# Kernel tuning notes

Hardware: AMD Instinct MI355X
Metric: run time of the kernel (lower is better)

Reference implementation:

```python
import jax, jax.numpy as jnp
import numpy as np

L = 5          # num_layer
H = 32         # num_heads (feature dim)
G = 32         # n_graph
NN = 256       # n_node per graph
KB = 8         # adjacency band half-width
N = G * (2 * (KB * NN - KB * (KB + 1) // 2))   # 128768 angle-graph nodes
E = N * 16                                      # 2060288 angle-graph edges
NRBF = 20
BN_EPS = 1e-5
GAMMA = 10.0


def _band_adj():
    i = np.arange(NN)
    d = np.abs(i[:, None] - i[None, :])
    a = (d <= KB) & (d > 0)
    return jnp.asarray(np.broadcast_to(a, (G, NN, NN)).copy())


def setup_inputs() -> dict:
    key = jax.random.key(0)
    ks = jax.random.split(key, 10)
    adj = _band_adj()
    x_mask = jnp.ones((G, NN), dtype=bool)
    x_3d = jax.random.uniform(ks[0], (N, 1), minval=0.8, maxval=1.8)
    edge_attr_3d = jax.random.uniform(ks[1], (E, 1), minval=0.0, maxval=float(np.pi))
    edge_index = jax.random.randint(ks[2], (2, E), 0, N)
    s1 = 1.0 / np.sqrt(NRBF)
    sH = 1.0 / np.sqrt(H)
    s2H = 1.0 / np.sqrt(2 * H)
    return {
        "x_3d": x_3d, "edge_attr_3d": edge_attr_3d,
        "edge_index": edge_index, "adj": adj, "x_mask": x_mask,
        "w_len": jax.random.normal(ks[3], (NRBF, H)) * s1, "b_len": jnp.zeros(H),
        "w_ang": jax.random.normal(ks[4], (NRBF, H)) * s1, "b_ang": jnp.zeros(H),
        "w1": jax.random.normal(ks[5], (L, H, 2 * H)) * sH, "b1": jnp.zeros((L, 2 * H)),
        "bn1_g": jnp.ones((L, 2 * H)), "bn1_b": jnp.zeros((L, 2 * H)),
        "w2": jax.random.normal(ks[6], (L, 2 * H, H)) * s2H, "b2": jnp.zeros((L, H)),
        "eps_gin": jnp.zeros(L),
        "bn_g": jnp.ones((L, H)), "bn_b": jnp.zeros((L, H)),
        "ln_g": jnp.ones(H), "ln_b": jnp.zeros(H),
    }


def _bn(h, g, b):
    # BatchNorm1d in training mode (batch statistics)
    m = jnp.mean(h, axis=0)
    v = jnp.var(h, axis=0)
    return (h - m) * jax.lax.rsqrt(v + BN_EPS) * g + b


def _rbf(x, centers):
    # x: [M,1] -> [M, NRBF]
    return jnp.exp(-GAMMA * (x - centers) ** 2)


def _forward(x_3d, edge_attr_3d, edge_index, adj,
             w_len, b_len, w_ang, b_ang,
             w1, b1, bn1_g, bn1_b, w2, b2, eps_gin, bn_g, bn_b, ln_g, ln_b):
    cen_len = jnp.arange(NRBF, dtype=x_3d.dtype) * 0.1           # bond length RBF centers
    cen_ang = jnp.linspace(0.0, np.pi, NRBF).astype(x_3d.dtype)  # bond angle RBF centers
    x = _rbf(x_3d, cen_len) @ w_len + b_len                      # [N,H]
    ea = _rbf(edge_attr_3d, cen_ang) @ w_ang + b_ang             # [E,H]
    src, dst = edge_index[0], edge_index[1]

    h = x
    for l in range(L):
        # GINConvBondAngle: message = relu(x_j + edge_attr); aggr = add
        msg = jax.nn.relu(h[src] + ea)                           # [E,H]
        agg = jax.ops.segment_sum(msg, dst, num_segments=N)      # [N,H]
        z = (1.0 + eps_gin[l]) * h + agg
        z = _bn(z @ w1[l] + b1[l], bn1_g[l], bn1_b[l])           # mlp Linear+BN
        z = jax.nn.relu(z) @ w2[l] + b2[l]                       # mlp ReLU+Linear
        h = _bn(z, bn_g[l], bn_b[l])                             # outer batch norm
        if l != L - 1:
            h = jax.nn.relu(h)
        # dropout p=0 -> identity; residual=False; JK='last'

    mu = jnp.mean(h, axis=-1, keepdims=True)
    var = jnp.var(h, axis=-1, keepdims=True)
    nr = (h - mu) * jax.lax.rsqrt(var + BN_EPS) * ln_g + ln_b    # LayerNorm, [N,H]

    # masked dense scatter into [G*NN*NN, H]
    eye = jnp.eye(NN, dtype=bool)
    mask = (adj & ~eye).reshape(-1)                              # exactly N Trues
    pos = jnp.cumsum(mask) - 1                                   # row in nr for each True
    out = jnp.where(mask[:, None], nr[jnp.clip(pos, 0, N - 1)], 0.0)
    return out.reshape(G, NN, NN, H).transpose(0, 3, 1, 2)       # [G,H,NN,NN]


def reference(x_3d, edge_attr_3d, edge_index, adj, x_mask,
              w_len, b_len, w_ang, b_ang,
              w1, b1, bn1_g, bn1_b, w2, b2, eps_gin, bn_g, bn_b, ln_g, ln_b):
    return _forward(x_3d, edge_attr_3d, edge_index, adj,
                    w_len, b_len, w_ang, b_ang,
                    w1, b1, bn1_g, bn1_b, w2, b2, eps_gin, bn_g, bn_b, ln_g, ln_b)
```

## Files before the change

### kernel.cpp

```cpp
#include <hip/hip_runtime.h>
#include <hip/hip_bf16.h>

using bf16 = __hip_bfloat16;

#define HH 32
#define HH2 64
#define NRBF_ 20
#define NL 5
#define NNN 256
#define KBW 8
#define PGN 4024
#define TTAB 4096
constexpr int NNODE = 128768;
constexpr int NEDGE = 2060288;
constexpr float BNEPS = 1e-5f;
constexpr float PI_F = 3.14159265358979323846f;

__global__ void __launch_bounds__(256) k_node_embed(const float* __restrict__ x3d,
                                                    const float* __restrict__ wlen,
                                                    const float* __restrict__ blen,
                                                    float* __restrict__ hbuf) {
  __shared__ float wl[NRBF_ * HH];
  __shared__ float bl[HH];
  int t = threadIdx.x;
  for (int j = t; j < NRBF_ * HH; j += 256) wl[j] = wlen[j];
  if (t < HH) bl[t] = blen[t];
  __syncthreads();
  int idx = blockIdx.x * 256 + t;
  int n = idx >> 5, c = idx & 31;
  float x = x3d[n];
  float acc = bl[c];
#pragma unroll
  for (int k = 0; k < NRBF_; ++k) {
    float d = x - 0.1f * (float)k;
    acc = fmaf(__expf(-10.f * d * d), wl[k * HH + c], acc);
  }
  hbuf[idx] = acc;
}

__global__ void __launch_bounds__(256) k_tab(const float* __restrict__ wang,
                                             const float* __restrict__ bang,
                                             float* __restrict__ tab) {
  __shared__ float wa[NRBF_ * HH];
  __shared__ float ba[HH];
  int t = threadIdx.x;
  for (int j = t; j < NRBF_ * HH; j += 256) wa[j] = wang[j];
  if (t < HH) ba[t] = bang[t];
  __syncthreads();
  int idx = blockIdx.x * 256 + t;
  int row = idx >> 5, c = idx & 31;
  float ang = (float)row * (PI_F / (float)(TTAB - 1));
  const float step = PI_F / 19.f;
  float acc = ba[c];
#pragma unroll
  for (int k = 0; k < NRBF_; ++k) {
    float d = ang - step * (float)k;
    acc = fmaf(__expf(-10.f * d * d), wa[k * HH + c], acc);
  }
  tab[row * HH + c] = acc;
}

__global__ void __launch_bounds__(256) k_hist(const int* __restrict__ dst, int* __restrict__ counts) {
  int e = blockIdx.x * 256 + threadIdx.x;
  atomicAdd(&counts[dst[e]], 1);
}

__global__ void __launch_bounds__(256) k_scan1(const int* __restrict__ counts, int* __restrict__ bsum) {
  __shared__ int sd[256];
  int t = threadIdx.x;
  sd[t] = counts[blockIdx.x * 256 + t];
  __syncthreads();
  for (int s = 128; s > 0; s >>= 1) { if (t < s) sd[t] += sd[t + s]; __syncthreads(); }
  if (t == 0) bsum[blockIdx.x] = sd[0];
}

__global__ void __launch_bounds__(512) k_scan2(const int* __restrict__ bsum, int* __restrict__ boff) {
  __shared__ int sd[512];
  int t = threadIdx.x;
  int v = (t < 503) ? bsum[t] : 0;
  sd[t] = v;
  __syncthreads();
  for (int off = 1; off < 512; off <<= 1) {
    int x = (t >= off) ? sd[t - off] : 0;
    __syncthreads();
    sd[t] += x;
    __syncthreads();
  }
  if (t < 503) boff[t] = sd[t] - v;
}

__global__ void __launch_bounds__(256) k_scan3(const int* __restrict__ counts, const int* __restrict__ boff,
                                               int* __restrict__ rowptr, int* __restrict__ cursor) {
  __shared__ int sd[256];
  int t = threadIdx.x;
  int i = blockIdx.x * 256 + t;
  int v = counts[i];
  sd[t] = v;
  __syncthreads();
  for (int off = 1; off < 256; off <<= 1) {
    int x = (t >= off) ? sd[t - off] : 0;
    __syncthreads();
    sd[t] += x;
    __syncthreads();
  }
  int excl = sd[t] - v + boff[blockIdx.x];
  rowptr[i] = excl;
  cursor[i] = excl;
  if (i == NNODE - 1) rowptr[NNODE] = excl + v;
}

__global__ void __launch_bounds__(256) k_scatter(const int* __restrict__ srcA,
                                                 const int* __restrict__ dstA,
                                                 const float* __restrict__ eattr,
                                                 int* __restrict__ cursor,
                                                 int2* __restrict__ pk) {
  int bid = blockIdx.x;
  int x = bid & 7;
  int j = bid >> 3;
  int lo = x * (NNODE / 8);
  int hi = lo + (NNODE / 8);
  int e0 = j * 2048 + threadIdx.x;
#pragma unroll
  for (int k = 0; k < 8; ++k) {
    int e = e0 + k * 256;
    int d = dstA[e];
    if (d >= lo && d < hi) {
      int pos = atomicAdd(&cursor[d], 1);
      pk[pos] = make_int2(srcA[e], __float_as_int(eattr[e]));
    }
  }
}

__global__ void __launch_bounds__(256) k_layerA(const float* __restrict__ hbuf,
                                                const int* __restrict__ rowptr,
                                                const int2* __restrict__ pk,
                                                const float* __restrict__ tab,
                                                const float* __restrict__ statsC,
                                                const float* __restrict__ bng,
                                                const float* __restrict__ bnb,
                                                const float* __restrict__ w1g,
                                                const float* __restrict__ b1g,
                                                const float* __restrict__ epsg,
                                                float* __restrict__ y1buf,
                                                float* __restrict__ statsA,
                                                int l, int relu) {
  __shared__ float w1s[HH * HH2];
  __shared__ float b1s[HH2];
  __shared__ float affs[HH], affsh[HH];
  __shared__ float tb[8][HH + 1];
  __shared__ float ps[HH2], pq[HH2];
  int t = threadIdx.x;
  const float* w1l = w1g + l * HH * HH2;
  for (int j = t; j < HH * HH2; j += 256) w1s[j] = w1l[j];
  if (t < HH2) { b1s[t] = b1g[l * HH2 + t]; ps[t] = 0.f; pq[t] = 0.f; }
  if (t < HH) {
    if (l == 0) { affs[t] = 1.f; affsh[t] = 0.f; }
    else {
      float sum = statsC[(l - 1) * 64 + t], sq = statsC[(l - 1) * 64 + 32 + t];
      float mean = sum / (float)NNODE;
      float var = fmaxf(sq / (float)NNODE - mean * mean, 0.f);
      float s = bng[(l - 1) * HH + t] * rsqrtf(var + BNEPS);
      affs[t] = s; affsh[t] = bnb[(l - 1) * HH + t] - mean * s;
    }
  }
  int g = t >> 5, c = t & 31;
  float epsv = 1.f + epsg[l];
  float lo = relu ? 0.f : -3.4e38f;
  const float angsc = (float)(TTAB - 1) / PI_F;
  float s0a = 0.f, s0q = 0.f, s1a = 0.f, s1q = 0.f;
  __syncthreads();
  float sc = affs[c], sh = affsh[c];
  int stride = gridDim.x * 8;
  int iters = (NNODE + stride - 1) / stride;
  int n = blockIdx.x * 8 + g;
  for (int it = 0; it < iters; ++it, n += stride) {
    bool val = n < NNODE;
    float tv = 0.f;
    if (val) {
      int p0 = rowptr[n], p1 = rowptr[n + 1];
      float hn = fmaxf(fmaf(hbuf[n * HH + c], sc, sh), lo);
      float acc = 0.f;
      int p = p0;
      for (; p + 8 <= p1; p += 8) {
        int2 q0 = pk[p], q1 = pk[p + 1], q2 = pk[p + 2], q3 = pk[p + 3];
        int2 q4 = pk[p + 4], q5 = pk[p + 5], q6 = pk[p + 6], q7 = pk[p + 7];
        float h0 = hbuf[q0.x * HH + c], h1 = hbuf[q1.x * HH + c];
        float h2 = hbuf[q2.x * HH + c], h3 = hbuf[q3.x * HH + c];
        float h4 = hbuf[q4.x * HH + c], h5 = hbuf[q5.x * HH + c];
        float h6 = hbuf[q6.x * HH + c], h7 = hbuf[q7.x * HH + c];
        int i0 = min((int)fmaf(__int_as_float(q0.y), angsc, 0.5f), TTAB - 1);
        int i1 = min((int)fmaf(__int_as_float(q1.y), angsc, 0.5f), TTAB - 1);
        int i2 = min((int)fmaf(__int_as_float(q2.y), angsc, 0.5f), TTAB - 1);
        int i3 = min((int)fmaf(__int_as_float(q3.y), angsc, 0.5f), TTAB - 1);
        int i4 = min((int)fmaf(__int_as_float(q4.y), angsc, 0.5f), TTAB - 1);
        int i5 = min((int)fmaf(__int_as_float(q5.y), angsc, 0.5f), TTAB - 1);
        int i6 = min((int)fmaf(__int_as_float(q6.y), angsc, 0.5f), TTAB - 1);
        int i7 = min((int)fmaf(__int_as_float(q7.y), angsc, 0.5f), TTAB - 1);
        float e0 = tab[i0 * HH + c], e1 = tab[i1 * HH + c];
        float e2 = tab[i2 * HH + c], e3 = tab[i3 * HH + c];
        float e4 = tab[i4 * HH + c], e5 = tab[i5 * HH + c];
        float e6 = tab[i6 * HH + c], e7 = tab[i7 * HH + c];
        h0 = fmaxf(fmaf(h0, sc, sh), lo); h1 = fmaxf(fmaf(h1, sc, sh), lo);
        h2 = fmaxf(fmaf(h2, sc, sh), lo); h3 = fmaxf(fmaf(h3, sc, sh), lo);
        h4 = fmaxf(fmaf(h4, sc, sh), lo); h5 = fmaxf(fmaf(h5, sc, sh), lo);
        h6 = fmaxf(fmaf(h6, sc, sh), lo); h7 = fmaxf(fmaf(h7, sc, sh), lo);
        acc += fmaxf(h0 + e0, 0.f) + fmaxf(h1 + e1, 0.f) + fmaxf(h2 + e2, 0.f) + fmaxf(h3 + e3, 0.f)
             + fmaxf(h4 + e4, 0.f) + fmaxf(h5 + e5, 0.f) + fmaxf(h6 + e6, 0.f) + fmaxf(h7 + e7, 0.f);
      }
      for (; p < p1; ++p) {
        int2 q0 = pk[p];
        float h0 = fmaxf(fmaf(hbuf[q0.x * HH + c], sc, sh), lo);
        int i0 = min((int)fmaf(__int_as_float(q0.y), angsc, 0.5f), TTAB - 1);
        acc += fmaxf(h0 + tab[i0 * HH + c], 0.f);
      }
      tv = fmaf(epsv, hn, acc);
    }
    tb[g][c] = tv;
    __builtin_amdgcn_wave_barrier();
    if (val) {
      float y0 = b1s[c], y1 = b1s[HH + c];
#pragma unroll
      for (int k = 0; k < HH; ++k) {
        float tk = tb[g][k];
        y0 = fmaf(tk, w1s[k * HH2 + c], y0);
        y1 = fmaf(tk, w1s[k * HH2 + HH + c], y1);
      }
      y1buf[n * HH2 + c] = y0;
      y1buf[n * HH2 + HH + c] = y1;
      s0a += y0; s0q += y0 * y0; s1a += y1; s1q += y1 * y1;
    }
    __builtin_amdgcn_wave_barrier();
  }
  s0a += __shfl_xor(s0a, 32); s0q += __shfl_xor(s0q, 32);
  s1a += __shfl_xor(s1a, 32); s1q += __shfl_xor(s1q, 32);
  if ((t & 32) == 0) {
    atomicAdd(&ps[c], s0a); atomicAdd(&pq[c], s0q);
    atomicAdd(&ps[HH + c], s1a); atomicAdd(&pq[HH + c], s1q);
  }
  __syncthreads();
  if (t < HH2) {
    atomicAdd(&statsA[l * 128 + t], ps[t]);
    atomicAdd(&statsA[l * 128 + 64 + t], pq[t]);
  }
}

__global__ void __launch_bounds__(256) k_layerC(const float* __restrict__ y1buf,
                                                const float* __restrict__ statsA,
                                                const float* __restrict__ g1,
                                                const float* __restrict__ bb1,
                                                const float* __restrict__ w2g,
                                                const float* __restrict__ b2g,
                                                float* __restrict__ hbuf,
                                                float* __restrict__ statsC, int l) {
  __shared__ float w2s[HH2 * HH];
  __shared__ float b2s[HH];
  __shared__ float a1s[HH2], a1sh[HH2];
  __shared__ float ab[8][HH2 + 1];
  __shared__ float ps[HH], pq[HH];
  int t = threadIdx.x;
  const float* w2l = w2g + l * HH2 * HH;
  for (int j = t; j < HH2 * HH; j += 256) w2s[j] = w2l[j];
  if (t < HH) { b2s[t] = b2g[l * HH + t]; ps[t] = 0.f; pq[t] = 0.f; }
  if (t < HH2) {
    float sum = statsA[l * 128 + t], sq = statsA[l * 128 + 64 + t];
    float mean = sum / (float)NNODE;
    float var = fmaxf(sq / (float)NNODE - mean * mean, 0.f);
    float s = g1[l * HH2 + t] * rsqrtf(var + BNEPS);
    a1s[t] = s; a1sh[t] = bb1[l * HH2 + t] - mean * s;
  }
  int g = t >> 5, c = t & 31;
  float sa = 0.f, sq = 0.f;
  __syncthreads();
  int stride = gridDim.x * 8;
  int iters = (NNODE + stride - 1) / stride;
  int n = blockIdx.x * 8 + g;
  for (int it = 0; it < iters; ++it, n += stride) {
    bool val = n < NNODE;
    float a0 = 0.f, a1 = 0.f;
    if (val) {
      a0 = fmaf(y1buf[n * HH2 + c], a1s[c], a1sh[c]);
      a1 = fmaf(y1buf[n * HH2 + HH + c], a1s[HH + c], a1sh[HH + c]);
    }
    ab[g][c] = fmaxf(a0, 0.f);
    ab[g][HH + c] = fmaxf(a1, 0.f);
    __builtin_amdgcn_wave_barrier();
    if (val) {
      float z = b2s[c];
#pragma unroll
      for (int k = 0; k < HH2; ++k) z = fmaf(ab[g][k], w2s[k * HH + c], z);
      hbuf[n * HH + c] = z;
      sa += z; sq += z * z;
    }
    __builtin_amdgcn_wave_barrier();
  }
  sa += __shfl_xor(sa, 32); sq += __shfl_xor(sq, 32);
  if ((t & 32) == 0) { atomicAdd(&ps[c], sa); atomicAdd(&pq[c], sq); }
  __syncthreads();
  if (t < HH) {
    atomicAdd(&statsC[l * 64 + t], ps[t]);
    atomicAdd(&statsC[l * 64 + 32 + t], pq[t]);
  }
}

__global__ void __launch_bounds__(256) k_output(const float* __restrict__ hbuf,
                                                const float* __restrict__ statsC,
                                                const float* __restrict__ bng,
                                                const float* __restrict__ bnb,
                                                const float* __restrict__ lng,
                                                const float* __restrict__ lnb,
                                                float* __restrict__ out) {
  __shared__ float nrb[16 * 33];
  __shared__ float affs[HH], affsh[HH];
  int t = threadIdx.x;
  if (t < HH) {
    float sum = statsC[(NL - 1) * 64 + t], sq = statsC[(NL - 1) * 64 + 32 + t];
    float mean = sum / (float)NNODE;
    float var = fmaxf(sq / (float)NNODE - mean * mean, 0.f);
    float s = bng[(NL - 1) * HH + t] * rsqrtf(var + BNEPS);
    affs[t] = s; affsh[t] = bnb[(NL - 1) * HH + t] - mean * s;
  }
  __syncthreads();
  int gi = blockIdx.x;
  int g = gi >> 8, i = gi & 255;
  int jlo = (i - KBW > 0) ? i - KBW : 0;
  int jhi = (i + KBW < NNN - 1) ? i + KBW : NNN - 1;
  int cnt = jhi - jlo;
  int Ai = (i <= 8) ? i * (i - 1) / 2 : 28 + 8 * (i - 8);
  int Bi = (i <= 248) ? 8 * i : 2012 - (256 - i) * (255 - i) / 2;
  int nb = g * PGN + Ai + Bi;
  int r = t >> 5, c = t & 31;
  float sc = affs[c], sh = affsh[c];
  float lg = lng[c], lb = lnb[c];
  for (int rr = r; rr < cnt; rr += 8) {
    float v = fmaf(hbuf[(nb + rr) * HH + c], sc, sh);
    float s = v;
#pragma unroll
    for (int off = 16; off > 0; off >>= 1) s += __shfl_xor(s, off, 32);
    float mean = s * (1.f / 32.f);
    float d = v - mean;
    float q = d * d;
#pragma unroll
    for (int off = 16; off > 0; off >>= 1) q += __shfl_xor(q, off, 32);
    float var = q * (1.f / 32.f);
    nrb[rr * 33 + c] = d * rsqrtf(var + BNEPS) * lg + lb;
  }
  __syncthreads();
  int j = t;
  bool valid = (j >= jlo) & (j <= jhi) & (j != i);
  int rr = j - jlo - ((j > i) ? 1 : 0);
  rr = (rr < 0) ? 0 : ((rr > 15) ? 15 : rr);
  size_t ob = (((size_t)g * HH) * NNN + i) * NNN + j;
#pragma unroll
  for (int h = 0; h < HH; ++h) {
    float val = valid ? nrb[rr * 33 + h] : 0.f;
    __builtin_nontemporal_store(val, &out[ob + (size_t)h * NNN * NNN]);
  }
}

extern "C" void kernel_launch(void* const* d_in, const int* in_sizes, int n_in,
                              void* d_out, int out_size, void* d_ws, size_t ws_size,
                              hipStream_t stream) {
  (void)in_sizes; (void)n_in;
  const float* x3d   = (const float*)d_in[0];
  const float* eattr = (const float*)d_in[1];
  const int*   eidx  = (const int*)d_in[2];
  const float* wlen = (const float*)d_in[5];
  const float* blen = (const float*)d_in[6];
  const float* wang = (const float*)d_in[7];
  const float* bang = (const float*)d_in[8];
  const float* w1g  = (const float*)d_in[9];
  const float* b1g  = (const float*)d_in[10];
  const float* g1   = (const float*)d_in[11];
  const float* bb1  = (const float*)d_in[12];
  const float* w2g  = (const float*)d_in[13];
  const float* b2g  = (const float*)d_in[14];
  const float* epsg = (const float*)d_in[15];
  const float* bng  = (const float*)d_in[16];
  const float* bnb  = (const float*)d_in[17];
  const float* lng  = (const float*)d_in[18];
  const float* lnb  = (const float*)d_in[19];
  float* out = (float*)d_out;

  char* ws = (char*)d_ws;
  size_t off = 0;
  auto alloc = [&](size_t bytes) {
    void* p = ws + off;
    off += (bytes + 255) & ~(size_t)255;
    return p;
  };
  int2*  pk         = (int2*)alloc((size_t)NEDGE * 8);
  int*   rowptr     = (int*)alloc((size_t)(NNODE + 1) * 4);
  int*   counts     = (int*)alloc((size_t)NNODE * 4);
  int*   cursor     = (int*)alloc((size_t)NNODE * 4);
  float* hbuf       = (float*)alloc((size_t)NNODE * HH * 4);
  float* y1buf      = (float*)alloc((size_t)NNODE * HH2 * 4);
  float* tab        = (float*)alloc((size_t)TTAB * HH * 4);
  float* statsA     = (float*)alloc(NL * 128 * 4);
  float* statsC     = (float*)alloc(NL * 64 * 4);
  int*   bsum       = (int*)alloc(503 * 4);
  int*   boff       = (int*)alloc(503 * 4);

  if (off > ws_size) {
    hipMemsetAsync(d_out, 0x7F, (size_t)out_size * 4, stream);
    return;
  }

  hipMemsetAsync(counts, 0, (size_t)NNODE * 4, stream);
  hipMemsetAsync(statsA, 0, NL * 128 * 4, stream);
  hipMemsetAsync(statsC, 0, NL * 64 * 4, stream);

  k_node_embed<<<NNODE * HH / 256, 256, 0, stream>>>(x3d, wlen, blen, hbuf);
  k_tab<<<TTAB * HH / 256, 256, 0, stream>>>(wang, bang, tab);
  k_hist<<<NEDGE / 256, 256, 0, stream>>>(eidx + NEDGE, counts);
  k_scan1<<<NNODE / 256, 256, 0, stream>>>(counts, bsum);
  k_scan2<<<1, 512, 0, stream>>>(bsum, boff);
  k_scan3<<<NNODE / 256, 256, 0, stream>>>(counts, boff, rowptr, cursor);
  k_scatter<<<8048, 256, 0, stream>>>(eidx, eidx + NEDGE, eattr, cursor, pk);

  for (int l = 0; l < NL; ++l) {
    k_layerA<<<2048, 256, 0, stream>>>(hbuf, rowptr, pk, tab, statsC, bng, bnb,
                                       w1g, b1g, epsg, y1buf, statsA, l, l >= 1 ? 1 : 0);
    k_layerC<<<2048, 256, 0, stream>>>(y1buf, statsA, g1, bb1, w2g, b2g, hbuf, statsC, l);
  }

  k_output<<<NNN * 32, 256, 0, stream>>>(hbuf, statsC, bng, bnb, lng, lnb, out);
}
```

Measured before the change: 1.124 ms.

## Store node features, angle table, and MLP activations in fp16; pack edge records

Node features, the angle embedding table and the first-MLP activations are now stored as fp16 instead of fp32. Edge records are packed into one 32-bit word holding a 17-bit source index and a precomputed 12-bit table index, and are read with nontemporal loads. The goal is to cut the memory traffic of the gather-heavy aggregation and of the layer passes. The cost is reduced precision in intermediate activations, and the packing assumes fewer than 2^17 nodes.

```diff
diff --git a/kernel.cpp b/kernel.cpp
--- a/kernel.cpp
+++ b/kernel.cpp
@@ -1,7 +1,6 @@
 #include <hip/hip_runtime.h>
 #include <hip/hip_bf16.h>
-
-using bf16 = __hip_bfloat16;
+#include <hip/hip_fp16.h>
 
 #define HH 32
 #define HH2 64
@@ -19,7 +18,7 @@
 __global__ void __launch_bounds__(256) k_node_embed(const float* __restrict__ x3d,
                                                     const float* __restrict__ wlen,
                                                     const float* __restrict__ blen,
-                                                    float* __restrict__ hbuf) {
+                                                    __half* __restrict__ hbuf) {
   __shared__ float wl[NRBF_ * HH];
   __shared__ float bl[HH];
   int t = threadIdx.x;
@@ -35,12 +34,12 @@
     float d = x - 0.1f * (float)k;
     acc = fmaf(__expf(-10.f * d * d), wl[k * HH + c], acc);
   }
-  hbuf[idx] = acc;
+  hbuf[idx] = __float2half(acc);
 }
 
 __global__ void __launch_bounds__(256) k_tab(const float* __restrict__ wang,
                                              const float* __restrict__ bang,
-                                             float* __restrict__ tab) {
+                                             __half* __restrict__ tab) {
   __shared__ float wa[NRBF_ * HH];
   __shared__ float ba[HH];
   int t = threadIdx.x;
@@ -57,7 +56,7 @@
     float d = ang - step * (float)k;
     acc = fmaf(__expf(-10.f * d * d), wa[k * HH + c], acc);
   }
-  tab[row * HH + c] = acc;
+  tab[row * HH + c] = __float2half(acc);
 }
 
 __global__ void __launch_bounds__(256) k_hist(const int* __restrict__ dst, int* __restrict__ counts) {
@@ -113,7 +112,8 @@
                                                  const int* __restrict__ dstA,
                                                  const float* __restrict__ eattr,
                                                  int* __restrict__ cursor,
-                                                 int2* __restrict__ pk) {
+                                                 unsigned int* __restrict__ pk) {
+  const float angsc = (float)(TTAB - 1) / PI_F;
   int bid = blockIdx.x;
   int x = bid & 7;
   int j = bid >> 3;
@@ -126,22 +126,23 @@
     int d = dstA[e];
     if (d >= lo && d < hi) {
       int pos = atomicAdd(&cursor[d], 1);
-      pk[pos] = make_int2(srcA[e], __float_as_int(eattr[e]));
-    }
-  }
-}
-
-__global__ void __launch_bounds__(256) k_layerA(const float* __restrict__ hbuf,
+      unsigned int idx = min((unsigned int)fmaf(eattr[e], angsc, 0.5f), (unsigned int)(TTAB - 1));
+      pk[pos] = (unsigned int)srcA[e] | (idx << 17);
+    }
+  }
+}
+
+__global__ void __launch_bounds__(256) k_layerA(const __half* __restrict__ hbuf,
                                                 const int* __restrict__ rowptr,
-                                                const int2* __restrict__ pk,
-                                                const float* __restrict__ tab,
+                                                const unsigned int* __restrict__ pk,
+                                                const __half* __restrict__ tab,
                                                 const float* __restrict__ statsC,
                                                 const float* __restrict__ bng,
                                                 const float* __restrict__ bnb,
                                                 const float* __restrict__ w1g,
                                                 const float* __restrict__ b1g,
                                                 const float* __restrict__ epsg,
-                                                float* __restrict__ y1buf,
+                                                __half* __restrict__ y1buf,
                                                 float* __restrict__ statsA,
                                                 int l, int relu) {
   __shared__ float w1s[HH * HH2];
@@ -166,7 +167,6 @@
   int g = t >> 5, c = t & 31;
   float epsv = 1.f + epsg[l];
   float lo = relu ? 0.f : -3.4e38f;
-  const float angsc = (float)(TTAB - 1) / PI_F;
   float s0a = 0.f, s0q = 0.f, s1a = 0.f, s1q = 0.f;
   __syncthreads();
   float sc = affs[c], sh = affsh[c];
@@ -178,28 +178,34 @@
     float tv = 0.f;
     if (val) {
       int p0 = rowptr[n], p1 = rowptr[n + 1];
-      float hn = fmaxf(fmaf(hbuf[n * HH + c], sc, sh), lo);
+      float hn = fmaxf(fmaf(__half2float(hbuf[n * HH + c]), sc, sh), lo);
       float acc = 0.f;
       int p = p0;
       for (; p + 8 <= p1; p += 8) {
-        int2 q0 = pk[p], q1 = pk[p + 1], q2 = pk[p + 2], q3 = pk[p + 3];
-        int2 q4 = pk[p + 4], q5 = pk[p + 5], q6 = pk[p + 6], q7 = pk[p + 7];
-        float h0 = hbuf[q0.x * HH + c], h1 = hbuf[q1.x * HH + c];
-        float h2 = hbuf[q2.x * HH + c], h3 = hbuf[q3.x * HH + c];
-        float h4 = hbuf[q4.x * HH + c], h5 = hbuf[q5.x * HH + c];
-        float h6 = hbuf[q6.x * HH + c], h7 = hbuf[q7.x * HH + c];
-        int i0 = min((int)fmaf(__int_as_float(q0.y), angsc, 0.5f), TTAB - 1);
-        int i1 = min((int)fmaf(__int_as_float(q1.y), angsc, 0.5f), TTAB - 1);
-        int i2 = min((int)fmaf(__int_as_float(q2.y), angsc, 0.5f), TTAB - 1);
-        int i3 = min((int)fmaf(__int_as_float(q3.y), angsc, 0.5f), TTAB - 1);
-        int i4 = min((int)fmaf(__int_as_float(q4.y), angsc, 0.5f), TTAB - 1);
-        int i5 = min((int)fmaf(__int_as_float(q5.y), angsc, 0.5f), TTAB - 1);
-        int i6 = min((int)fmaf(__int_as_float(q6.y), angsc, 0.5f), TTAB - 1);
-        int i7 = min((int)fmaf(__int_as_float(q7.y), angsc, 0.5f), TTAB - 1);
-        float e0 = tab[i0 * HH + c], e1 = tab[i1 * HH + c];
-        float e2 = tab[i2 * HH + c], e3 = tab[i3 * HH + c];
-        float e4 = tab[i4 * HH + c], e5 = tab[i5 * HH + c];
-        float e6 = tab[i6 * HH + c], e7 = tab[i7 * HH + c];
+        unsigned int q0 = __builtin_nontemporal_load(&pk[p]);
+        unsigned int q1 = __builtin_nontemporal_load(&pk[p + 1]);
+        unsigned int q2 = __builtin_nontemporal_load(&pk[p + 2]);
+        unsigned int q3 = __builtin_nontemporal_load(&pk[p + 3]);
+        unsigned int q4 = __builtin_nontemporal_load(&pk[p + 4]);
+        unsigned int q5 = __builtin_nontemporal_load(&pk[p + 5]);
+        unsigned int q6 = __builtin_nontemporal_load(&pk[p + 6]);
+        unsigned int q7 = __builtin_nontemporal_load(&pk[p + 7]);
+        float h0 = __half2float(hbuf[(q0 & 0x1FFFF) * HH + c]);
+        float h1 = __half2float(hbuf[(q1 & 0x1FFFF) * HH + c]);
+        float h2 = __half2float(hbuf[(q2 & 0x1FFFF) * HH + c]);
+        float h3 = __half2float(hbuf[(q3 & 0x1FFFF) * HH + c]);
+        float h4 = __half2float(hbuf[(q4 & 0x1FFFF) * HH + c]);
+        float h5 = __half2float(hbuf[(q5 & 0x1FFFF) * HH + c]);
+        float h6 = __half2float(hbuf[(q6 & 0x1FFFF) * HH + c]);
+        float h7 = __half2float(hbuf[(q7 & 0x1FFFF) * HH + c]);
+        float e0 = __half2float(tab[(q0 >> 17) * HH + c]);
+        float e1 = __half2float(tab[(q1 >> 17) * HH + c]);
+        float e2 = __half2float(tab[(q2 >> 17) * HH + c]);
+        float e3 = __half2float(tab[(q3 >> 17) * HH + c]);
+        float e4 = __half2float(tab[(q4 >> 17) * HH + c]);
+        float e5 = __half2float(tab[(q5 >> 17) * HH + c]);
+        float e6 = __half2float(tab[(q6 >> 17) * HH + c]);
+        float e7 = __half2float(tab[(q7 >> 17) * HH + c]);
         h0 = fmaxf(fmaf(h0, sc, sh), lo); h1 = fmaxf(fmaf(h1, sc, sh), lo);
         h2 = fmaxf(fmaf(h2, sc, sh), lo); h3 = fmaxf(fmaf(h3, sc, sh), lo);
         h4 = fmaxf(fmaf(h4, sc, sh), lo); h5 = fmaxf(fmaf(h5, sc, sh), lo);
@@ -208,10 +214,9 @@
              + fmaxf(h4 + e4, 0.f) + fmaxf(h5 + e5, 0.f) + fmaxf(h6 + e6, 0.f) + fmaxf(h7 + e7, 0.f);
       }
       for (; p < p1; ++p) {
-        int2 q0 = pk[p];
-        float h0 = fmaxf(fmaf(hbuf[q0.x * HH + c], sc, sh), lo);
-        int i0 = min((int)fmaf(__int_as_float(q0.y), angsc, 0.5f), TTAB - 1);
-        acc += fmaxf(h0 + tab[i0 * HH + c], 0.f);
+        unsigned int q0 = __builtin_nontemporal_load(&pk[p]);
+        float h0 = fmaxf(fmaf(__half2float(hbuf[(q0 & 0x1FFFF) * HH + c]), sc, sh), lo);
+        acc += fmaxf(h0 + __half2float(tab[(q0 >> 17) * HH + c]), 0.f);
       }
       tv = fmaf(epsv, hn, acc);
     }
@@ -225,9 +230,11 @@
         y0 = fmaf(tk, w1s[k * HH2 + c], y0);
         y1 = fmaf(tk, w1s[k * HH2 + HH + c], y1);
       }
-      y1buf[n * HH2 + c] = y0;
-      y1buf[n * HH2 + HH + c] = y1;
-      s0a += y0; s0q += y0 * y0; s1a += y1; s1q += y1 * y1;
+      __half hy0 = __float2half(y0), hy1 = __float2half(y1);
+      y1buf[n * HH2 + c] = hy0;
+      y1buf[n * HH2 + HH + c] = hy1;
+      float z0 = __half2float(hy0), z1 = __half2float(hy1);
+      s0a += z0; s0q += z0 * z0; s1a += z1; s1q += z1 * z1;
     }
     __builtin_amdgcn_wave_barrier();
   }
@@ -244,13 +251,13 @@
   }
 }
 
-__global__ void __launch_bounds__(256) k_layerC(const float* __restrict__ y1buf,
+__global__ void __launch_bounds__(256) k_layerC(const __half* __restrict__ y1buf,
                                                 const float* __restrict__ statsA,
                                                 const float* __restrict__ g1,
                                                 const float* __restrict__ bb1,
                                                 const float* __restrict__ w2g,
                                                 const float* __restrict__ b2g,
-                                                float* __restrict__ hbuf,
+                                                __half* __restrict__ hbuf,
                                                 float* __restrict__ statsC, int l) {
   __shared__ float w2s[HH2 * HH];
   __shared__ float b2s[HH];
@@ -278,8 +285,8 @@
     bool val = n < NNODE;
     float a0 = 0.f, a1 = 0.f;
     if (val) {
-      a0 = fmaf(y1buf[n * HH2 + c], a1s[c], a1sh[c]);
-      a1 = fmaf(y1buf[n * HH2 + HH + c], a1s[HH + c], a1sh[HH + c]);
+      a0 = fmaf(__half2float(y1buf[n * HH2 + c]), a1s[c], a1sh[c]);
+      a1 = fmaf(__half2float(y1buf[n * HH2 + HH + c]), a1s[HH + c], a1sh[HH + c]);
     }
     ab[g][c] = fmaxf(a0, 0.f);
     ab[g][HH + c] = fmaxf(a1, 0.f);
@@ -288,8 +295,10 @@
       float z = b2s[c];
 #pragma unroll
       for (int k = 0; k < HH2; ++k) z = fmaf(ab[g][k], w2s[k * HH + c], z);
-      hbuf[n * HH + c] = z;
-      sa += z; sq += z * z;
+      __half zh = __float2half(z);
+      hbuf[n * HH + c] = zh;
+      float zq = __half2float(zh);
+      sa += zq; sq += zq * zq;
     }
     __builtin_amdgcn_wave_barrier();
   }
@@ -302,7 +311,7 @@
   }
 }
 
-__global__ void __launch_bounds__(256) k_output(const float* __restrict__ hbuf,
+__global__ void __launch_bounds__(256) k_output(const __half* __restrict__ hbuf,
                                                 const float* __restrict__ statsC,
                                                 const float* __restrict__ bng,
                                                 const float* __restrict__ bnb,
@@ -332,7 +341,7 @@
   float sc = affs[c], sh = affsh[c];
   float lg = lng[c], lb = lnb[c];
   for (int rr = r; rr < cnt; rr += 8) {
-    float v = fmaf(hbuf[(nb + rr) * HH + c], sc, sh);
+    float v = fmaf(__half2float(hbuf[(nb + rr) * HH + c]), sc, sh);
     float s = v;
 #pragma unroll
     for (int off = 16; off > 0; off >>= 1) s += __shfl_xor(s, off, 32);
@@ -388,13 +397,13 @@
     off += (bytes + 255) & ~(size_t)255;
     return p;
   };
-  int2*  pk         = (int2*)alloc((size_t)NEDGE * 8);
+  unsigned int* pk  = (unsigned int*)alloc((size_t)NEDGE * 4);
   int*   rowptr     = (int*)alloc((size_t)(NNODE + 1) * 4);
   int*   counts     = (int*)alloc((size_t)NNODE * 4);
   int*   cursor     = (int*)alloc((size_t)NNODE * 4);
-  float* hbuf       = (float*)alloc((size_t)NNODE * HH * 4);
-  float* y1buf      = (float*)alloc((size_t)NNODE * HH2 * 4);
-  float* tab        = (float*)alloc((size_t)TTAB * HH * 4);
+  __half* hbuf      = (__half*)alloc((size_t)NNODE * HH * 2);
+  __half* y1buf     = (__half*)alloc((size_t)NNODE * HH2 * 2);
+  __half* tab       = (__half*)alloc((size_t)TTAB * HH * 2);
   float* statsA     = (float*)alloc(NL * 128 * 4);
   float* statsC     = (float*)alloc(NL * 64 * 4);
   int*   bsum       = (int*)alloc(503 * 4);
```

Result: no change. 1.144 ms (+1.7%).
